# Performance work log

Hardware: AMD Instinct MI355X
Metric: run time of the kernel (lower is better)

Reference implementation:

```python
import jax, jax.numpy as jnp
import numpy as np

# Instant-NGP HashGrid constants (match tcnn encoding_config defaults in the module)
N_LEVELS = 16
N_FEATS = 2
LOG2_T = 16
T = 1 << LOG2_T            # hashmap entries per level
BASE_RES = 16
PER_LEVEL_SCALE = 1.5
N_POINTS = 1 << 20
PRIMES = (1, 2654435761, 805459861)  # tcnn spatial-hash primes

# 8 corner offsets of the unit cube, [8,3]
_CORNERS = np.array([[i, j, k] for i in (0, 1) for j in (0, 1) for k in (0, 1)], dtype=np.float32)


def setup_inputs() -> dict:
    key = jax.random.key(0)
    k1, k2 = jax.random.split(key)
    x = jax.random.uniform(k1, (N_POINTS, 3), dtype=jnp.float32)
    # tcnn initializes hash tables uniform in [-1e-4, 1e-4]
    table = jax.random.uniform(k2, (N_LEVELS, T, N_FEATS), minval=-1e-4, maxval=1e-4, dtype=jnp.float32)
    return {"x": x, "table": table}


def _corner_index(grid, res, dense):
    # grid: [N,8,3] int32 corner coordinates -> [N,8] table index
    if dense:
        g = jnp.clip(grid, 0, res - 1)
        return g[..., 0] + g[..., 1] * res + g[..., 2] * res * res
    g = grid.astype(jnp.uint32)
    h = (g[..., 0] * jnp.uint32(PRIMES[0])
         ^ g[..., 1] * jnp.uint32(PRIMES[1])
         ^ g[..., 2] * jnp.uint32(PRIMES[2]))
    return (h & jnp.uint32(T - 1)).astype(jnp.int32)


def _hashgrid_forward(x, table):
    x = x.astype(jnp.float32)
    offs = jnp.asarray(_CORNERS)                      # [8,3]
    outs = []
    for level in range(N_LEVELS):
        # tcnn: grid_scale = base * s^level - 1 ; resolution = ceil(scale)+1
        scale = float(BASE_RES * (PER_LEVEL_SCALE ** level) - 1.0)
        res = int(np.ceil(scale)) + 1
        dense = res ** 3 <= T                          # tcnn uses dense indexing when the grid fits
        pos = x * scale + 0.5                          # [N,3]
        g0 = jnp.floor(pos)
        frac = pos - g0                                # [N,3] trilinear fractions
        grid = (g0[:, None, :] + offs[None]).astype(jnp.int32)   # [N,8,3]
        idx = _corner_index(grid, res, dense)          # [N,8]
        feat = table[level][idx]                       # [N,8,F] irregular gather
        # trilinear weights: prod over dims of frac or (1-frac) per corner
        w = jnp.prod(jnp.where(offs[None] > 0, frac[:, None, :], 1.0 - frac[:, None, :]), axis=-1)  # [N,8]
        outs.append(jnp.sum(w[..., None] * feat, axis=1))        # [N,F]
    return jnp.concatenate(outs, axis=-1)              # [N, L*F] = [N,32]


def reference(x, table):
    return _hashgrid_forward(x, table)
```

## Files before the change

### kernel.cpp

```cpp
#include <hip/hip_runtime.h>
#include <stdint.h>


#define NLVL 16
#define TS 65536
#define P2 2654435761u
#define P3 805459861u

typedef float v4f __attribute__((ext_vector_type(4)));
typedef float v2f __attribute__((ext_vector_type(2)));
typedef float v4fa8 __attribute__((ext_vector_type(4), aligned(8)));

__constant__ float C_SCALES[NLVL] = {
    15.0f, 23.0f, 35.0f, 53.0f, 80.0f, 120.5f, 181.25f, 272.375f,
    409.0625f, 614.09375f, 921.640625f, 1382.9609375f,
    2074.94140625f, 3112.912109375f, 4669.8681640625f, 7005.30224609375f};

__device__ __forceinline__ v2f v4lo(v4f v) { v2f r; r.x = v.x; r.y = v.y; return r; }
__device__ __forceinline__ v2f v4hi(v4f v) { v2f r; r.x = v.z; r.y = v.w; return r; }
__device__ __forceinline__ v2f v4lo8(v4fa8 v) { v2f r; r.x = v.x; r.y = v.y; return r; }
__device__ __forceinline__ v2f v4hi8(v4fa8 v) { v2f r; r.x = v.z; r.y = v.w; return r; }

__device__ __forceinline__ void lds_put2(float* s, int p, int gl, int h,
                                         float a, float b) {
    const int slot = (gl + p) & 3;
    const int a32 = p * 16 + slot * 4 + h * 2;
    s[a32] = a;
    s[a32 + 1] = b;
}

__device__ __forceinline__ v2f hashed_level(float px, float py, float pz,
                                            float scale, const v2f* tbl) {
    const float fx = px * scale + 0.5f;
    const float fy = py * scale + 0.5f;
    const float fz = pz * scale + 0.5f;
    const float gx = floorf(fx), gy = floorf(fy), gz = floorf(fz);
    const float wx = fx - gx, wy = fy - gy, wz = fz - gz;
    const int ix = (int)gx, iy = (int)gy, iz = (int)gz;

    const uint32_t bx = (uint32_t)ix;
    const uint32_t hy0 = (uint32_t)iy * P2, hy1 = hy0 + P2;
    const uint32_t hz0 = (uint32_t)iz * P3, hz1 = hz0 + P3;
    const uint32_t b00 = hy0 ^ hz0, b01 = hy0 ^ hz1;
    const uint32_t b10 = hy1 ^ hz0, b11 = hy1 ^ hz1;
    const uint32_t i00 = (bx ^ b00) & (TS - 1);
    const uint32_t i01 = (bx ^ b01) & (TS - 1);
    const uint32_t i10 = (bx ^ b10) & (TS - 1);
    const uint32_t i11 = (bx ^ b11) & (TS - 1);
    const v4f* tbl4 = (const v4f*)tbl;
    const v4f f00 = tbl4[i00 >> 1];
    const v4f f01 = tbl4[i01 >> 1];
    const v4f f10 = tbl4[i10 >> 1];
    const v4f f11 = tbl4[i11 >> 1];
    const v2f c0 = (i00 & 1) ? v4hi(f00) : v4lo(f00);
    const v2f c1 = (i01 & 1) ? v4hi(f01) : v4lo(f01);
    const v2f c2 = (i10 & 1) ? v4hi(f10) : v4lo(f10);
    const v2f c3 = (i11 & 1) ? v4hi(f11) : v4lo(f11);
    v2f c4, c5, c6, c7;
    if ((ix & 1) == 0) {
        c4 = (i00 & 1) ? v4lo(f00) : v4hi(f00);
        c5 = (i01 & 1) ? v4lo(f01) : v4hi(f01);
        c6 = (i10 & 1) ? v4lo(f10) : v4hi(f10);
        c7 = (i11 & 1) ? v4lo(f11) : v4hi(f11);
    } else {
        const uint32_t bx1 = bx + 1;
        c4 = tbl[(bx1 ^ b00) & (TS - 1)];
        c5 = tbl[(bx1 ^ b01) & (TS - 1)];
        c6 = tbl[(bx1 ^ b10) & (TS - 1)];
        c7 = tbl[(bx1 ^ b11) & (TS - 1)];
    }

    const float ux = 1.0f - wx, uy = 1.0f - wy, uz = 1.0f - wz;
    const float w0 = ux * uy * uz, w1 = ux * uy * wz;
    const float w2 = ux * wy * uz, w3 = ux * wy * wz;
    const float w4 = wx * uy * uz, w5 = wx * uy * wz;
    const float w6 = wx * wy * uz, w7 = wx * wy * wz;

    v2f o;
    o.x = w0 * c0.x + w1 * c1.x + w2 * c2.x + w3 * c3.x +
          w4 * c4.x + w5 * c5.x + w6 * c6.x + w7 * c7.x;
    o.y = w0 * c0.y + w1 * c1.y + w2 * c2.y + w3 * c3.y +
          w4 * c4.y + w5 * c5.y + w6 * c6.y + w7 * c7.y;
    return o;
}

__global__ __launch_bounds__(256, 8) void hashgrid_fwd(
    const float* __restrict__ x,
    const float* __restrict__ table,
    float* __restrict__ out,
    int n)
{
    __shared__ float s_out[256 * 16];

    const int tid0 = blockIdx.x * 256 + threadIdx.x;
    const int tid = min(tid0, n - 1);
    const int p = threadIdx.x;

    const float px = x[3 * tid + 0];
    const float py = x[3 * tid + 1];
    const float pz = x[3 * tid + 2];

    v4f* outb4 = (v4f*)out + (size_t)blockIdx.x * (256 * 8);
    const long long lim4 = (long long)n * 8 - (long long)blockIdx.x * (256 * 8);

    {
        const int RESO[3] = {16, 24, 36};
        const float DSC[3] = {15.0f, 23.0f, 35.0f};
#pragma unroll
        for (int l = 0; l < 3; ++l) {
            const float scale = DSC[l];
            const float fx = px * scale + 0.5f;
            const float fy = py * scale + 0.5f;
            const float fz = pz * scale + 0.5f;
            const float gx = floorf(fx), gy = floorf(fy), gz = floorf(fz);
            const float wx = fx - gx, wy = fy - gy, wz = fz - gz;
            const int ix = (int)gx, iy = (int)gy, iz = (int)gz;

            const v2f* tbl = ((const v2f*)table) + (size_t)l * TS;
            const int R = RESO[l];
            const int x0 = min(ix, R - 1);
            const int y0 = min(iy, R - 1), y1 = min(iy + 1, R - 1);
            const int z0 = min(iz, R - 1), z1 = min(iz + 1, R - 1);
            const int xb = min(x0, R - 2);
            const bool hi0 = (x0 != xb);
            const int y0R = y0 * R, y1R = y1 * R;
            const int z0R = z0 * R * R, z1R = z1 * R * R;
            const v4fa8 f00 = *(const v4fa8*)(tbl + (xb + y0R + z0R));
            const v4fa8 f01 = *(const v4fa8*)(tbl + (xb + y0R + z1R));
            const v4fa8 f10 = *(const v4fa8*)(tbl + (xb + y1R + z0R));
            const v4fa8 f11 = *(const v4fa8*)(tbl + (xb + y1R + z1R));
            const v2f c0 = hi0 ? v4hi8(f00) : v4lo8(f00), c4 = v4hi8(f00);
            const v2f c1 = hi0 ? v4hi8(f01) : v4lo8(f01), c5 = v4hi8(f01);
            const v2f c2 = hi0 ? v4hi8(f10) : v4lo8(f10), c6 = v4hi8(f10);
            const v2f c3 = hi0 ? v4hi8(f11) : v4lo8(f11), c7 = v4hi8(f11);

            const float ux = 1.0f - wx, uy = 1.0f - wy, uz = 1.0f - wz;
            const float w0 = ux * uy * uz, w1 = ux * uy * wz;
            const float w2 = ux * wy * uz, w3 = ux * wy * wz;
            const float w4 = wx * uy * uz, w5 = wx * uy * wz;
            const float w6 = wx * wy * uz, w7 = wx * wy * wz;

            const float o0 = w0 * c0.x + w1 * c1.x + w2 * c2.x + w3 * c3.x +
                             w4 * c4.x + w5 * c5.x + w6 * c6.x + w7 * c7.x;
            const float o1 = w0 * c0.y + w1 * c1.y + w2 * c2.y + w3 * c3.y +
                             w4 * c4.y + w5 * c5.y + w6 * c6.y + w7 * c7.y;
            lds_put2(s_out, p, l >> 1, l & 1, o0, o1);
        }
    }
#pragma unroll
    for (int l = 3; l < 8; ++l) {
        const v2f o = hashed_level(px, py, pz, C_SCALES[l],
                                   ((const v2f*)table) + (size_t)l * TS);
        lds_put2(s_out, p, l >> 1, l & 1, o.x, o.y);
    }
    __syncthreads();
#pragma unroll
    for (int r = 0; r < 4; ++r) {
        const int e = r * 256 + threadIdx.x;
        const int pp = e >> 2, g = e & 3;
        const int slot = (g + pp) & 3;
        const v4f v = *(const v4f*)&s_out[pp * 16 + slot * 4];
        const int o4 = pp * 8 + g;
        if (o4 < lim4) outb4[o4] = v;
    }
    __syncthreads();

#pragma unroll
    for (int l = 8; l < NLVL; ++l) {
        const v2f o = hashed_level(px, py, pz, C_SCALES[l],
                                   ((const v2f*)table) + (size_t)l * TS);
        lds_put2(s_out, p, (l >> 1) - 4, l & 1, o.x, o.y);
    }
    __syncthreads();
#pragma unroll
    for (int r = 0; r < 4; ++r) {
        const int e = r * 256 + threadIdx.x;
        const int pp = e >> 2, g = e & 3;
        const int slot = (g + pp) & 3;
        const v4f v = *(const v4f*)&s_out[pp * 16 + slot * 4];
        const int o4 = pp * 8 + 4 + g;
        if (o4 < lim4) outb4[o4] = v;
    }
}

extern "C" void kernel_launch(void* const* d_in, const int* in_sizes, int n_in,
                              void* d_out, int out_size, void* d_ws, size_t ws_size,
                              hipStream_t stream) {
    const float* x = (const float*)d_in[0];
    const float* table = (const float*)d_in[1];
    float* out = (float*)d_out;
    const int n = in_sizes[0] / 3;
    const int block = 256;
    const int grid = (n + block - 1) / block;
    hashgrid_fwd<<<grid, block, 0, stream>>>(x, table, out, n);
}
```

Baseline: 504.5 us.

## Software-pipeline hashed level gathers three levels ahead and store output once

Splits each hashed level into an issue phase, which computes the hashes and launches all eight gathers, and a consume phase, which does the trilinear blend. A rotating set of three level states keeps gathers for upcoming levels in flight while earlier levels are blended. It drops the even-x 16-byte pair-load trick in favour of eight plain 8-byte gathers per level. The shared buffer doubles so all 32 outputs are written in a single pass with one barrier, and launch bounds drop from 8 to 4 blocks to make room for the extra live registers, which lowers occupancy.

```diff
diff --git a/kernel.cpp b/kernel.cpp
--- a/kernel.cpp
+++ b/kernel.cpp
@@ -16,81 +16,70 @@
     409.0625f, 614.09375f, 921.640625f, 1382.9609375f,
     2074.94140625f, 3112.912109375f, 4669.8681640625f, 7005.30224609375f};
 
-__device__ __forceinline__ v2f v4lo(v4f v) { v2f r; r.x = v.x; r.y = v.y; return r; }
-__device__ __forceinline__ v2f v4hi(v4f v) { v2f r; r.x = v.z; r.y = v.w; return r; }
 __device__ __forceinline__ v2f v4lo8(v4fa8 v) { v2f r; r.x = v.x; r.y = v.y; return r; }
 __device__ __forceinline__ v2f v4hi8(v4fa8 v) { v2f r; r.x = v.z; r.y = v.w; return r; }
 
-__device__ __forceinline__ void lds_put2(float* s, int p, int gl, int h,
+__device__ __forceinline__ void lds_put2(float* s, int p, int l,
                                          float a, float b) {
+    const int t = l >> 3;
+    const int gl = (l >> 1) & 3;
     const int slot = (gl + p) & 3;
-    const int a32 = p * 16 + slot * 4 + h * 2;
+    const int a32 = t * 4096 + p * 16 + slot * 4 + (l & 1) * 2;
     s[a32] = a;
     s[a32 + 1] = b;
 }
 
-__device__ __forceinline__ v2f hashed_level(float px, float py, float pz,
-                                            float scale, const v2f* tbl) {
+struct LvlS {
+    v2f c0, c1, c2, c3, c4, c5, c6, c7;
+    float wx, wy, wz;
+};
+
+__device__ __forceinline__ void lvl_issue(LvlS& s, float px, float py,
+                                          float pz, float scale,
+                                          const v2f* __restrict__ tbl) {
     const float fx = px * scale + 0.5f;
     const float fy = py * scale + 0.5f;
     const float fz = pz * scale + 0.5f;
     const float gx = floorf(fx), gy = floorf(fy), gz = floorf(fz);
-    const float wx = fx - gx, wy = fy - gy, wz = fz - gz;
-    const int ix = (int)gx, iy = (int)gy, iz = (int)gz;
-
-    const uint32_t bx = (uint32_t)ix;
-    const uint32_t hy0 = (uint32_t)iy * P2, hy1 = hy0 + P2;
-    const uint32_t hz0 = (uint32_t)iz * P3, hz1 = hz0 + P3;
+    s.wx = fx - gx;
+    s.wy = fy - gy;
+    s.wz = fz - gz;
+    const uint32_t bx = (uint32_t)(int)gx, bx1 = bx + 1;
+    const uint32_t hy0 = (uint32_t)(int)gy * P2, hy1 = hy0 + P2;
+    const uint32_t hz0 = (uint32_t)(int)gz * P3, hz1 = hz0 + P3;
     const uint32_t b00 = hy0 ^ hz0, b01 = hy0 ^ hz1;
     const uint32_t b10 = hy1 ^ hz0, b11 = hy1 ^ hz1;
-    const uint32_t i00 = (bx ^ b00) & (TS - 1);
-    const uint32_t i01 = (bx ^ b01) & (TS - 1);
-    const uint32_t i10 = (bx ^ b10) & (TS - 1);
-    const uint32_t i11 = (bx ^ b11) & (TS - 1);
-    const v4f* tbl4 = (const v4f*)tbl;
-    const v4f f00 = tbl4[i00 >> 1];
-    const v4f f01 = tbl4[i01 >> 1];
-    const v4f f10 = tbl4[i10 >> 1];
-    const v4f f11 = tbl4[i11 >> 1];
-    const v2f c0 = (i00 & 1) ? v4hi(f00) : v4lo(f00);
-    const v2f c1 = (i01 & 1) ? v4hi(f01) : v4lo(f01);
-    const v2f c2 = (i10 & 1) ? v4hi(f10) : v4lo(f10);
-    const v2f c3 = (i11 & 1) ? v4hi(f11) : v4lo(f11);
-    v2f c4, c5, c6, c7;
-    if ((ix & 1) == 0) {
-        c4 = (i00 & 1) ? v4lo(f00) : v4hi(f00);
-        c5 = (i01 & 1) ? v4lo(f01) : v4hi(f01);
-        c6 = (i10 & 1) ? v4lo(f10) : v4hi(f10);
-        c7 = (i11 & 1) ? v4lo(f11) : v4hi(f11);
-    } else {
-        const uint32_t bx1 = bx + 1;
-        c4 = tbl[(bx1 ^ b00) & (TS - 1)];
-        c5 = tbl[(bx1 ^ b01) & (TS - 1)];
-        c6 = tbl[(bx1 ^ b10) & (TS - 1)];
-        c7 = tbl[(bx1 ^ b11) & (TS - 1)];
-    }
+    s.c0 = tbl[(bx ^ b00) & (TS - 1)];
+    s.c1 = tbl[(bx ^ b01) & (TS - 1)];
+    s.c2 = tbl[(bx ^ b10) & (TS - 1)];
+    s.c3 = tbl[(bx ^ b11) & (TS - 1)];
+    s.c4 = tbl[(bx1 ^ b00) & (TS - 1)];
+    s.c5 = tbl[(bx1 ^ b01) & (TS - 1)];
+    s.c6 = tbl[(bx1 ^ b10) & (TS - 1)];
+    s.c7 = tbl[(bx1 ^ b11) & (TS - 1)];
+}
 
-    const float ux = 1.0f - wx, uy = 1.0f - wy, uz = 1.0f - wz;
-    const float w0 = ux * uy * uz, w1 = ux * uy * wz;
-    const float w2 = ux * wy * uz, w3 = ux * wy * wz;
-    const float w4 = wx * uy * uz, w5 = wx * uy * wz;
-    const float w6 = wx * wy * uz, w7 = wx * wy * wz;
-
+__device__ __forceinline__ v2f lvl_consume(const LvlS& s) {
+    const float ux = 1.0f - s.wx, uy = 1.0f - s.wy, uz = 1.0f - s.wz;
+    const float w0 = ux * uy * uz, w1 = ux * uy * s.wz;
+    const float w2 = ux * s.wy * uz, w3 = ux * s.wy * s.wz;
+    const float w4 = s.wx * uy * uz, w5 = s.wx * uy * s.wz;
+    const float w6 = s.wx * s.wy * uz, w7 = s.wx * s.wy * s.wz;
     v2f o;
-    o.x = w0 * c0.x + w1 * c1.x + w2 * c2.x + w3 * c3.x +
-          w4 * c4.x + w5 * c5.x + w6 * c6.x + w7 * c7.x;
-    o.y = w0 * c0.y + w1 * c1.y + w2 * c2.y + w3 * c3.y +
-          w4 * c4.y + w5 * c5.y + w6 * c6.y + w7 * c7.y;
+    o.x = w0 * s.c0.x + w1 * s.c1.x + w2 * s.c2.x + w3 * s.c3.x +
+          w4 * s.c4.x + w5 * s.c5.x + w6 * s.c6.x + w7 * s.c7.x;
+    o.y = w0 * s.c0.y + w1 * s.c1.y + w2 * s.c2.y + w3 * s.c3.y +
+          w4 * s.c4.y + w5 * s.c5.y + w6 * s.c6.y + w7 * s.c7.y;
     return o;
 }
 
-__global__ __launch_bounds__(256, 8) void hashgrid_fwd(
+__global__ __launch_bounds__(256, 4) void hashgrid_fwd(
     const float* __restrict__ x,
     const float* __restrict__ table,
     float* __restrict__ out,
     int n)
 {
-    __shared__ float s_out[256 * 16];
+    __shared__ float s_out[256 * 32];
 
     const int tid0 = blockIdx.x * 256 + threadIdx.x;
     const int tid = min(tid0, n - 1);
@@ -102,6 +91,13 @@
 
     v4f* outb4 = (v4f*)out + (size_t)blockIdx.x * (256 * 8);
     const long long lim4 = (long long)n * 8 - (long long)blockIdx.x * (256 * 8);
+
+    const v2f* tblv = (const v2f*)table;
+
+    LvlS s0, s1, s2;
+    lvl_issue(s0, px, py, pz, C_SCALES[3], tblv + (size_t)3 * TS);
+    lvl_issue(s1, px, py, pz, C_SCALES[4], tblv + (size_t)4 * TS);
+    lvl_issue(s2, px, py, pz, C_SCALES[5], tblv + (size_t)5 * TS);
 
     {
         const int RESO[3] = {16, 24, 36};
@@ -116,7 +112,7 @@
             const float wx = fx - gx, wy = fy - gy, wz = fz - gz;
             const int ix = (int)gx, iy = (int)gy, iz = (int)gz;
 
-            const v2f* tbl = ((const v2f*)table) + (size_t)l * TS;
+            const v2f* tbl = tblv + (size_t)l * TS;
             const int R = RESO[l];
             const int x0 = min(ix, R - 1);
             const int y0 = min(iy, R - 1), y1 = min(iy + 1, R - 1);
@@ -144,41 +140,39 @@
                              w4 * c4.x + w5 * c5.x + w6 * c6.x + w7 * c7.x;
             const float o1 = w0 * c0.y + w1 * c1.y + w2 * c2.y + w3 * c3.y +
                              w4 * c4.y + w5 * c5.y + w6 * c6.y + w7 * c7.y;
-            lds_put2(s_out, p, l >> 1, l & 1, o0, o1);
+            lds_put2(s_out, p, l, o0, o1);
         }
     }
-#pragma unroll
-    for (int l = 3; l < 8; ++l) {
-        const v2f o = hashed_level(px, py, pz, C_SCALES[l],
-                                   ((const v2f*)table) + (size_t)l * TS);
-        lds_put2(s_out, p, l >> 1, l & 1, o.x, o.y);
-    }
-    __syncthreads();
-#pragma unroll
-    for (int r = 0; r < 4; ++r) {
-        const int e = r * 256 + threadIdx.x;
-        const int pp = e >> 2, g = e & 3;
-        const int slot = (g + pp) & 3;
-        const v4f v = *(const v4f*)&s_out[pp * 16 + slot * 4];
-        const int o4 = pp * 8 + g;
-        if (o4 < lim4) outb4[o4] = v;
-    }
+
+#define STEP(S, LCUR) { const v2f o = lvl_consume(S); lds_put2(s_out, p, LCUR, o.x, o.y); }
+#define REISSUE(S, LNXT) lvl_issue(S, px, py, pz, C_SCALES[LNXT], tblv + (size_t)(LNXT) * TS);
+
+    STEP(s0, 3)  REISSUE(s0, 6)
+    STEP(s1, 4)  REISSUE(s1, 7)
+    STEP(s2, 5)  REISSUE(s2, 8)
+    STEP(s0, 6)  REISSUE(s0, 9)
+    STEP(s1, 7)  REISSUE(s1, 10)
+    STEP(s2, 8)  REISSUE(s2, 11)
+    STEP(s0, 9)  REISSUE(s0, 12)
+    STEP(s1, 10) REISSUE(s1, 13)
+    STEP(s2, 11) REISSUE(s2, 14)
+    STEP(s0, 12) REISSUE(s0, 15)
+    STEP(s1, 13)
+    STEP(s2, 14)
+    STEP(s0, 15)
+#undef STEP
+#undef REISSUE
+
     __syncthreads();
 
 #pragma unroll
-    for (int l = 8; l < NLVL; ++l) {
-        const v2f o = hashed_level(px, py, pz, C_SCALES[l],
-                                   ((const v2f*)table) + (size_t)l * TS);
-        lds_put2(s_out, p, (l >> 1) - 4, l & 1, o.x, o.y);
-    }
-    __syncthreads();
-#pragma unroll
-    for (int r = 0; r < 4; ++r) {
+    for (int r = 0; r < 8; ++r) {
         const int e = r * 256 + threadIdx.x;
-        const int pp = e >> 2, g = e & 3;
+        const int pp = e >> 3, q = e & 7;
+        const int t = q >> 2, g = q & 3;
         const int slot = (g + pp) & 3;
-        const v4f v = *(const v4f*)&s_out[pp * 16 + slot * 4];
-        const int o4 = pp * 8 + 4 + g;
+        const v4f v = *(const v4f*)&s_out[t * 4096 + pp * 16 + slot * 4];
+        const int o4 = pp * 8 + q;
         if (o4 < lim4) outb4[o4] = v;
     }
 }
```

Result: slower. 600.5 us (+19.0%).
